# Kernel tuning notes

Measured on AMD Instinct MI355X. Metric: run time of the kernel, lower is better.

Reference implementation:

```python
import jax, jax.numpy as jnp
import numpy as np

B, T, D, E = 4, 2048, 1024, 8


def setup_inputs() -> dict:
    key = jax.random.key(0)
    ks = jax.random.split(key, 8)
    scale_g = float(np.sqrt(2.0 / (D + E)))  # xavier_uniform-ish scale for W_g
    scale_w = float(1.0 / np.sqrt(D))
    return {
        "x": jax.random.normal(ks[0], (B, T, D), dtype=jnp.float32),
        "noise": jax.random.normal(ks[1], (B, T, E), dtype=jnp.float32),  # the N(0,1) sample in Gating.forward
        "W_g": jax.random.normal(ks[2], (D, E), dtype=jnp.float32) * scale_g,
        "W_noise": jax.random.normal(ks[3], (D, E), dtype=jnp.float32),
        "W1": jax.random.normal(ks[4], (E, D, D), dtype=jnp.float32) * scale_w,
        "b1": jnp.zeros((E, D), dtype=jnp.float32),
        "W2": jax.random.normal(ks[5], (E, D, D), dtype=jnp.float32) * scale_w,
        "b2": jnp.zeros((E, D), dtype=jnp.float32),
        "k": 2,
    }


def _gates(x, noise, W_g, W_noise, k):
    # h = x@W_g + N(0,1) + softplus(x@W_noise)   (note: noise added, not scaled)
    h = jnp.einsum("btd,de->bte", x, W_g) + noise + jax.nn.softplus(
        jnp.einsum("btd,de->bte", x, W_noise)
    )
    kth = jax.lax.top_k(h, k)[0][..., -1:]           # kth largest per token
    h_masked = jnp.where(h >= kth, h, -jnp.inf)       # keepTopK (ties kept, as in torch)
    return jax.nn.softmax(h_masked, axis=-1)          # [B,T,E]


def reference(x, noise, W_g, W_noise, W1, b1, W2, b2, k):
    gates = _gates(x, noise, W_g, W_noise, k)
    # Dense loop over experts (faithful to original): every expert FFN on all tokens.
    # hidden: [E,B,T,D]
    hidden = jax.nn.relu(jnp.einsum("btd,edh->ebth", x, W1) + b1[:, None, None, :])
    expert_out = jnp.einsum("ebth,eho->ebto", hidden, W2) + b2[:, None, None, :]
    # mask-weighted combine: sum_e expert_out_e * gates[...,e]
    return jnp.einsum("ebtd,bte->btd", expert_out, gates)
```

## Files before the change

kernel.cpp:

```cpp
#include <hip/hip_runtime.h>
#include <hip/hip_bf16.h>

#define BTOK 8192
#define DDIM 1024
#define NEXP 8

typedef unsigned short u16;
typedef unsigned int u32;
typedef __attribute__((ext_vector_type(8))) short short8;
typedef __attribute__((ext_vector_type(4))) float f32x4;

constexpr int BM = 128, BN = 128, BK = 64;
constexpr int SLOTCAP = 3072;
constexpr int NT = DDIM / BK;

__device__ __forceinline__ u16 f2bf(float f){
  __hip_bfloat16 h = __float2bfloat16(f);
  return *reinterpret_cast<u16*>(&h);
}
__device__ __forceinline__ float bf2f(u16 v){
  return __uint_as_float(((u32)v) << 16);
}
__device__ __forceinline__ void gll16(const u16* gsrc, u16* ldst){
  __builtin_amdgcn_global_load_lds((const __attribute__((address_space(1))) void*)gsrc,
                                   (__attribute__((address_space(3))) void*)ldst,
                                   16, 0, 0);
}

#define GTOK 16
__global__ __launch_bounds__(512) void gating_kernel(
    const float* __restrict__ x, const float* __restrict__ noise,
    const float* __restrict__ Wg, const float* __restrict__ Wn,
    const int* __restrict__ kp,
    float* __restrict__ gates, int* __restrict__ counts, int* __restrict__ lists,
    int* __restrict__ tokmap, int* __restrict__ ncnt)
{
  __shared__ float lw[2][NEXP][4][260];
  __shared__ float lh[GTOK][NEXP];
  const int tid = threadIdx.x;

  for (int i = tid; i < 2*DDIM*NEXP; i += 512){
    const int mat = i >> 13;
    const int r   = i & 8191;
    const int d = r >> 3, ee = r & 7;
    const float* W = mat ? Wn : Wg;
    lw[mat][ee][d >> 8][d & 255] = W[r];
  }
  __syncthreads();

  const int q   = tid & 3;
  const int e   = (tid >> 2) & 7;
  const int tok = tid >> 5;
  const int t   = blockIdx.x * GTOK + tok;

  const float4* x4 = reinterpret_cast<const float4*>(x + (size_t)t*DDIM + q*256);
  const float4* g4 = reinterpret_cast<const float4*>(&lw[0][e][q][0]);
  const float4* n4 = reinterpret_cast<const float4*>(&lw[1][e][q][0]);
  float ag = 0.f, an = 0.f;
  #pragma unroll 8
  for (int j = 0; j < 64; ++j){
    const float4 xv = x4[j];
    const float4 wg = g4[j];
    const float4 wn = n4[j];
    ag = fmaf(xv.x,wg.x,fmaf(xv.y,wg.y,fmaf(xv.z,wg.z,fmaf(xv.w,wg.w,ag))));
    an = fmaf(xv.x,wn.x,fmaf(xv.y,wn.y,fmaf(xv.z,wn.z,fmaf(xv.w,wn.w,an))));
  }
  ag += __shfl_xor(ag, 1); an += __shfl_xor(an, 1);
  ag += __shfl_xor(ag, 2); an += __shfl_xor(an, 2);
  if (q == 0){
    const float sp = (an > 20.f) ? an : log1pf(expf(an));
    lh[tok][e] = ag + noise[(size_t)t*NEXP + e] + sp;
  }
  __syncthreads();
  if (tid < GTOK){
    const int tt = blockIdx.x * GTOK + tid;
    float h[NEXP];
    #pragma unroll
    for (int ee=0; ee<NEXP; ee++) h[ee] = lh[tid][ee];
    int kk = *kp; kk = kk<1?1:(kk>NEXP?NEXP:kk);
    bool used[NEXP];
    for (int ee=0; ee<NEXP; ee++) used[ee]=false;
    float kth = 0.f;
    for (int i2=0;i2<kk;i2++){
      int bi=0; float bv=-3.4e38f;
      for (int ee=0; ee<NEXP; ee++) if (!used[ee] && h[ee]>bv){bv=h[ee]; bi=ee;}
      used[bi]=true; kth=bv;
    }
    float m=-3.4e38f;
    for (int ee=0; ee<NEXP; ee++) if (h[ee]>=kth && h[ee]>m) m=h[ee];
    float p[NEXP], s=0.f;
    for (int ee=0; ee<NEXP; ee++){ p[ee]=(h[ee]>=kth)?expf(h[ee]-m):0.f; s+=p[ee]; }
    const float inv = 1.f/s;
    int nsel = 0;
    for (int ee=0; ee<NEXP; ee++){
      const float g = p[ee]*inv;
      gates[(size_t)tt*NEXP+ee] = g;
      if (g > 0.f){
        const int slot = atomicAdd(&counts[ee], 1);
        lists[ee*BTOK + slot] = tt;
        tokmap[tt*NEXP + nsel] = (ee << 13) | (slot & 8191);
        nsel++;
      }
    }
    ncnt[tt] = nsel;
  }
}

__global__ __launch_bounds__(256) void cast_x_kernel(const float4* __restrict__ x4,
                                                     ushort4* __restrict__ xb4)
{
  const int i = blockIdx.x*256 + threadIdx.x;
  const float4 v = x4[i];
  xb4[i] = make_ushort4(f2bf(v.x), f2bf(v.y), f2bf(v.z), f2bf(v.w));
}

__global__ __launch_bounds__(256) void trans_kernel(
    const float* __restrict__ W1, const float* __restrict__ W2,
    u16* __restrict__ W1T, u16* __restrict__ W2T)
{
  __shared__ float tile[64][65];
  const int mz = blockIdx.z;
  const float* src = (mz < NEXP) ? (W1  + (size_t)mz*DDIM*DDIM) : (W2  + (size_t)(mz-NEXP)*DDIM*DDIM);
  u16*       dst = (mz < NEXP) ? (W1T + (size_t)mz*DDIM*DDIM) : (W2T + (size_t)(mz-NEXP)*DDIM*DDIM);
  const int r0 = blockIdx.x*64, c0 = blockIdx.y*64;
  const int tx = threadIdx.x & 63, ty = threadIdx.x >> 6;
  #pragma unroll
  for (int i=ty;i<64;i+=4)
    tile[i][tx] = src[(size_t)(r0+i)*DDIM + c0+tx];
  __syncthreads();
  #pragma unroll
  for (int i=ty;i<64;i+=4)
    dst[(size_t)(c0+i)*DDIM + r0+tx] = f2bf(tile[tx][i]);
}

template<int LAYER>
__device__ __forceinline__ void ffn_body(
    const u16* __restrict__ Asrc, const u16* __restrict__ WT,
    const float* __restrict__ bias,
    const int* __restrict__ counts, const int* __restrict__ lists,
    u16* __restrict__ dst)
{
  const int e  = blockIdx.z;
  int cnt = counts[e]; if (cnt > SLOTCAP) cnt = SLOTCAP;
  const int m0 = blockIdx.x*BM;
  if (m0 >= cnt) return;
  const int n0 = blockIdx.y*BN;

  __shared__ __align__(16) u16 ldsA[2][BM*BK];
  __shared__ __align__(16) u16 ldsB[2][BN*BK];

  const int tid = threadIdx.x;
  const int wave = tid>>6, lane = tid&63;
  const int wm = wave>>1, wn = wave&1;

  const u16* aSrc[4]; const u16* bSrc[4];
  {
    const int lr = lane>>3, sp = lane&7;
    #pragma unroll
    for (int i=0;i<4;i++){
      const int row = wave*32 + i*8 + lr;
      const int ku  = sp ^ (row&7);
      size_t abase;
      if constexpr (LAYER==1){
        int gr = m0 + row; if (gr >= cnt) gr = cnt-1;
        const int tok = lists[e*BTOK + gr];
        abase = (size_t)tok * DDIM;
      } else {
        abase = ((size_t)e*SLOTCAP + m0 + row) * DDIM;
      }
      aSrc[i] = Asrc + abase + ku*8;
      bSrc[i] = WT + ((size_t)e*DDIM + n0 + row)*DDIM + ku*8;
    }
  }

  const int q = lane>>4, l16 = lane&15;
  int aoff[2][4], boff[2][4];
  #pragma unroll
  for (int f=0;f<4;f++){
    const int ra = wm*64 + f*16 + l16;
    const int rb = wn*64 + f*16 + l16;
    #pragma unroll
    for (int kk=0;kk<2;kk++){
      aoff[kk][f] = ra*BK + (((kk*4+q) ^ (ra&7))*8);
      boff[kk][f] = rb*BK + (((kk*4+q) ^ (rb&7))*8);
    }
  }

  f32x4 acc[4][4];
  #pragma unroll
  for (int i=0;i<4;i++)
    #pragma unroll
    for (int j=0;j<4;j++)
      acc[i][j] = (f32x4){0.f,0.f,0.f,0.f};

  #pragma unroll
  for (int i=0;i<4;i++){
    gll16(aSrc[i], &ldsA[0][(wave*4+i)*512]);
    gll16(bSrc[i], &ldsB[0][(wave*4+i)*512]);
  }
  __syncthreads();

  int cur = 0;
  for (int kt = 0; kt < NT-1; ++kt){
    #pragma unroll
    for (int i=0;i<4;i++){
      gll16(aSrc[i] + (size_t)(kt+1)*BK, &ldsA[cur^1][(wave*4+i)*512]);
      gll16(bSrc[i] + (size_t)(kt+1)*BK, &ldsB[cur^1][(wave*4+i)*512]);
    }
    #pragma unroll
    for (int kk=0;kk<2;kk++){
      short8 af[4], bfv[4];
      #pragma unroll
      for (int f=0;f<4;f++) af[f]  = *reinterpret_cast<const short8*>(&ldsA[cur][aoff[kk][f]]);
      #pragma unroll
      for (int f=0;f<4;f++) bfv[f] = *reinterpret_cast<const short8*>(&ldsB[cur][boff[kk][f]]);
      #pragma unroll
      for (int fm=0;fm<4;fm++)
        #pragma unroll
        for (int fn=0;fn<4;fn++)
          acc[fm][fn] = __builtin_amdgcn_mfma_f32_16x16x32_bf16(af[fm], bfv[fn], acc[fm][fn], 0, 0, 0);
    }
    __syncthreads();
    cur ^= 1;
  }
  #pragma unroll
  for (int kk=0;kk<2;kk++){
    short8 af[4], bfv[4];
    #pragma unroll
    for (int f=0;f<4;f++) af[f]  = *reinterpret_cast<const short8*>(&ldsA[cur][aoff[kk][f]]);
    #pragma unroll
    for (int f=0;f<4;f++) bfv[f] = *reinterpret_cast<const short8*>(&ldsB[cur][boff[kk][f]]);
    #pragma unroll
    for (int fm=0;fm<4;fm++)
      #pragma unroll
      for (int fn=0;fn<4;fn++)
        acc[fm][fn] = __builtin_amdgcn_mfma_f32_16x16x32_bf16(af[fm], bfv[fn], acc[fm][fn], 0, 0, 0);
  }

  #pragma unroll
  for (int fm=0;fm<4;fm++){
    #pragma unroll
    for (int r=0;r<4;r++){
      const int row = wm*64 + fm*16 + q*4 + r;
      const int gr  = m0 + row;
      #pragma unroll
      for (int fn=0;fn<4;fn++){
        const int col = n0 + wn*64 + fn*16 + l16;
        float v = acc[fm][fn][r] + bias[e*DDIM + col];
        if constexpr (LAYER==1) v = v > 0.f ? v : 0.f;
        dst[((size_t)e*SLOTCAP + gr)*DDIM + col] = f2bf(v);
      }
    }
  }
}

__global__ __launch_bounds__(256) void ffn1_kernel(
    const u16* __restrict__ A, const u16* __restrict__ WT, const float* __restrict__ b,
    const int* __restrict__ counts, const int* __restrict__ lists, u16* __restrict__ dst)
{ ffn_body<1>(A, WT, b, counts, lists, dst); }

__global__ __launch_bounds__(256) void ffn2_kernel(
    const u16* __restrict__ A, const u16* __restrict__ WT, const float* __restrict__ b,
    const int* __restrict__ counts, const int* __restrict__ lists, u16* __restrict__ dst)
{ ffn_body<2>(A, WT, b, counts, lists, dst); }

__global__ __launch_bounds__(256) void combine_kernel(
    const u16* __restrict__ partial, const int* __restrict__ tokmap,
    const int* __restrict__ ncnt, const float* __restrict__ gates,
    float* __restrict__ out)
{
  const int t = blockIdx.x, c = threadIdx.x;
  const int n = ncnt[t];
  float4 acc = {0.f, 0.f, 0.f, 0.f};
  for (int j = 0; j < n; ++j){
    const int ent  = tokmap[t*NEXP + j];
    const int e    = ent >> 13, slot = ent & 8191;
    if (slot >= SLOTCAP) continue;
    const float g = gates[(size_t)t*NEXP + e];
    const ushort4 pv = reinterpret_cast<const ushort4*>(
        partial + ((size_t)e*SLOTCAP + slot)*DDIM)[c];
    acc.x = fmaf(g, bf2f(pv.x), acc.x);
    acc.y = fmaf(g, bf2f(pv.y), acc.y);
    acc.z = fmaf(g, bf2f(pv.z), acc.z);
    acc.w = fmaf(g, bf2f(pv.w), acc.w);
  }
  reinterpret_cast<float4*>(out + (size_t)t*DDIM)[c] = acc;
}

extern "C" void kernel_launch(void* const* d_in, const int* in_sizes, int n_in,
                              void* d_out, int out_size, void* d_ws, size_t ws_size,
                              hipStream_t stream)
{
  const float* x     = (const float*)d_in[0];
  const float* noise = (const float*)d_in[1];
  const float* Wg    = (const float*)d_in[2];
  const float* Wn    = (const float*)d_in[3];
  const float* W1    = (const float*)d_in[4];
  const float* b1    = (const float*)d_in[5];
  const float* W2    = (const float*)d_in[6];
  const float* b2    = (const float*)d_in[7];
  const int*   kp    = (const int*)d_in[8];
  float* out = (float*)d_out;

  char* ws = (char*)d_ws;
  int*   counts = (int*)ws;
  int*   lists  = (int*)(ws + 4096);
  float* gates  = (float*)(ws + 266240);
  int*   tokmap = (int*)(ws + 528384);
  int*   ncnt   = (int*)(ws + 790528);
  u16*   xb     = (u16*)(ws + 1048576);
  u16*   W1T    = (u16*)(ws + 17825792);
  u16*   W2T    = (u16*)(ws + 34603008);
  u16*   hidden = (u16*)(ws + 51380224);
  u16*   partial= (u16*)(ws + 101711872);
  const size_t NEED = 152043520ull;

  hipMemsetAsync(counts, 0, 64, stream);
  if (ws_size < NEED){
    hipMemsetAsync(d_out, 0, (size_t)out_size*sizeof(float), stream);
    return;
  }

  cast_x_kernel<<<BTOK*DDIM/4/256, 256, 0, stream>>>((const float4*)x, (ushort4*)xb);
  trans_kernel<<<dim3(16,16,16), 256, 0, stream>>>(W1, W2, W1T, W2T);
  gating_kernel<<<BTOK/GTOK, 512, 0, stream>>>(x, noise, Wg, Wn, kp,
                                               gates, counts, lists, tokmap, ncnt);
  ffn1_kernel<<<dim3(SLOTCAP/BM, DDIM/BN, NEXP), 256, 0, stream>>>(
      xb, W1T, b1, counts, lists, hidden);
  ffn2_kernel<<<dim3(SLOTCAP/BM, DDIM/BN, NEXP), 256, 0, stream>>>(
      hidden, W2T, b2, counts, lists, partial);
  combine_kernel<<<BTOK, 256, 0, stream>>>(partial, tokmap, ncnt, gates, out);
}
```

Before: 366.6 us.

## Fuse bf16 cast of x into gating, split selection into block-aggregated kernel

The fp32-to-bf16 cast of x moves into the gating score kernel, so x is read from global memory once instead of twice, and one launch is removed. Top-k selection and slot assignment move to a separate kernel with one token per thread. Slots are counted first with shared-memory atomics and then reserved with one global atomic per expert per block. The gating dot products also use split accumulators for more ILP. In exchange there is an extra launch, a small h buffer round trip, and a divergent bf16 store done only by the e==0 lanes.

```diff
diff --git a/kernel.cpp b/kernel.cpp
--- a/kernel.cpp
+++ b/kernel.cpp
@@ -28,15 +28,12 @@
 }
 
 #define GTOK 16
-__global__ __launch_bounds__(512) void gating_kernel(
+__global__ __launch_bounds__(512) void gating_score_kernel(
     const float* __restrict__ x, const float* __restrict__ noise,
     const float* __restrict__ Wg, const float* __restrict__ Wn,
-    const int* __restrict__ kp,
-    float* __restrict__ gates, int* __restrict__ counts, int* __restrict__ lists,
-    int* __restrict__ tokmap, int* __restrict__ ncnt)
+    float* __restrict__ h_out, u16* __restrict__ xb)
 {
   __shared__ float lw[2][NEXP][4][260];
-  __shared__ float lh[GTOK][NEXP];
   const int tid = threadIdx.x;
 
   for (int i = tid; i < 2*DDIM*NEXP; i += 512){
@@ -56,62 +53,87 @@
   const float4* x4 = reinterpret_cast<const float4*>(x + (size_t)t*DDIM + q*256);
   const float4* g4 = reinterpret_cast<const float4*>(&lw[0][e][q][0]);
   const float4* n4 = reinterpret_cast<const float4*>(&lw[1][e][q][0]);
-  float ag = 0.f, an = 0.f;
+  ushort4* xb4 = reinterpret_cast<ushort4*>(xb + (size_t)t*DDIM + q*256);
+  float agx=0.f, agz=0.f, anx=0.f, anz=0.f;
   #pragma unroll 8
   for (int j = 0; j < 64; ++j){
     const float4 xv = x4[j];
     const float4 wg = g4[j];
     const float4 wn = n4[j];
-    ag = fmaf(xv.x,wg.x,fmaf(xv.y,wg.y,fmaf(xv.z,wg.z,fmaf(xv.w,wg.w,ag))));
-    an = fmaf(xv.x,wn.x,fmaf(xv.y,wn.y,fmaf(xv.z,wn.z,fmaf(xv.w,wn.w,an))));
-  }
+    agx = fmaf(xv.x,wg.x, fmaf(xv.y,wg.y, agx));
+    agz = fmaf(xv.z,wg.z, fmaf(xv.w,wg.w, agz));
+    anx = fmaf(xv.x,wn.x, fmaf(xv.y,wn.y, anx));
+    anz = fmaf(xv.z,wn.z, fmaf(xv.w,wn.w, anz));
+    if (e == 0)
+      xb4[j] = make_ushort4(f2bf(xv.x), f2bf(xv.y), f2bf(xv.z), f2bf(xv.w));
+  }
+  float ag = agx + agz, an = anx + anz;
   ag += __shfl_xor(ag, 1); an += __shfl_xor(an, 1);
   ag += __shfl_xor(ag, 2); an += __shfl_xor(an, 2);
   if (q == 0){
     const float sp = (an > 20.f) ? an : log1pf(expf(an));
-    lh[tok][e] = ag + noise[(size_t)t*NEXP + e] + sp;
-  }
-  __syncthreads();
-  if (tid < GTOK){
-    const int tt = blockIdx.x * GTOK + tid;
-    float h[NEXP];
-    #pragma unroll
-    for (int ee=0; ee<NEXP; ee++) h[ee] = lh[tid][ee];
-    int kk = *kp; kk = kk<1?1:(kk>NEXP?NEXP:kk);
-    bool used[NEXP];
-    for (int ee=0; ee<NEXP; ee++) used[ee]=false;
-    float kth = 0.f;
-    for (int i2=0;i2<kk;i2++){
-      int bi=0; float bv=-3.4e38f;
-      for (int ee=0; ee<NEXP; ee++) if (!used[ee] && h[ee]>bv){bv=h[ee]; bi=ee;}
-      used[bi]=true; kth=bv;
-    }
-    float m=-3.4e38f;
-    for (int ee=0; ee<NEXP; ee++) if (h[ee]>=kth && h[ee]>m) m=h[ee];
-    float p[NEXP], s=0.f;
-    for (int ee=0; ee<NEXP; ee++){ p[ee]=(h[ee]>=kth)?expf(h[ee]-m):0.f; s+=p[ee]; }
-    const float inv = 1.f/s;
-    int nsel = 0;
-    for (int ee=0; ee<NEXP; ee++){
-      const float g = p[ee]*inv;
-      gates[(size_t)tt*NEXP+ee] = g;
-      if (g > 0.f){
-        const int slot = atomicAdd(&counts[ee], 1);
-        lists[ee*BTOK + slot] = tt;
-        tokmap[tt*NEXP + nsel] = (ee << 13) | (slot & 8191);
-        nsel++;
-      }
-    }
-    ncnt[tt] = nsel;
-  }
-}
-
-__global__ __launch_bounds__(256) void cast_x_kernel(const float4* __restrict__ x4,
-                                                     ushort4* __restrict__ xb4)
-{
-  const int i = blockIdx.x*256 + threadIdx.x;
-  const float4 v = x4[i];
-  xb4[i] = make_ushort4(f2bf(v.x), f2bf(v.y), f2bf(v.z), f2bf(v.w));
+    h_out[(size_t)t*NEXP + e] = ag + noise[(size_t)t*NEXP + e] + sp;
+  }
+}
+
+__global__ __launch_bounds__(256) void gating_select_kernel(
+    const float* __restrict__ h_in, const int* __restrict__ kp,
+    float* __restrict__ gates, int* __restrict__ counts, int* __restrict__ lists,
+    int* __restrict__ tokmap, int* __restrict__ ncnt)
+{
+  __shared__ int lcnt[NEXP];
+  __shared__ int lbase[NEXP];
+  const int tid = threadIdx.x;
+  const int t   = blockIdx.x*256 + tid;
+  if (tid < NEXP) lcnt[tid] = 0;
+  __syncthreads();
+
+  float h[NEXP];
+  const float4 h0 = reinterpret_cast<const float4*>(h_in + (size_t)t*NEXP)[0];
+  const float4 h1 = reinterpret_cast<const float4*>(h_in + (size_t)t*NEXP)[1];
+  h[0]=h0.x; h[1]=h0.y; h[2]=h0.z; h[3]=h0.w;
+  h[4]=h1.x; h[5]=h1.y; h[6]=h1.z; h[7]=h1.w;
+
+  int kk = *kp; kk = kk<1?1:(kk>NEXP?NEXP:kk);
+  bool used[NEXP];
+  #pragma unroll
+  for (int e=0;e<NEXP;e++) used[e]=false;
+  float kth = 0.f;
+  for (int i=0;i<kk;i++){
+    int bi=0; float bv=-3.4e38f;
+    #pragma unroll
+    for (int e=0;e<NEXP;e++) if (!used[e] && h[e]>bv){bv=h[e]; bi=e;}
+    used[bi]=true; kth=bv;
+  }
+  float m=-3.4e38f;
+  #pragma unroll
+  for (int e=0;e<NEXP;e++) if (h[e]>=kth && h[e]>m) m=h[e];
+  float p[NEXP], s=0.f;
+  #pragma unroll
+  for (int e=0;e<NEXP;e++){ p[e]=(h[e]>=kth)?expf(h[e]-m):0.f; s+=p[e]; }
+  const float inv = 1.f/s;
+  float g[NEXP];
+  int lslot[NEXP];
+  #pragma unroll
+  for (int e=0;e<NEXP;e++){
+    g[e] = p[e]*inv;
+    gates[(size_t)t*NEXP + e] = g[e];
+    if (g[e] > 0.f) lslot[e] = atomicAdd(&lcnt[e], 1);
+  }
+  __syncthreads();
+  if (tid < NEXP) lbase[tid] = atomicAdd(&counts[tid], lcnt[tid]);
+  __syncthreads();
+  int idx = 0;
+  #pragma unroll
+  for (int e=0;e<NEXP;e++){
+    if (g[e] > 0.f){
+      const int slot = lbase[e] + lslot[e];
+      lists[e*BTOK + slot] = t;
+      tokmap[t*NEXP + idx] = (e << 13) | (slot & 8191);
+      idx++;
+    }
+  }
+  ncnt[t] = idx;
 }
 
 __global__ __launch_bounds__(256) void trans_kernel(
@@ -308,12 +330,13 @@
   float* gates  = (float*)(ws + 266240);
   int*   tokmap = (int*)(ws + 528384);
   int*   ncnt   = (int*)(ws + 790528);
-  u16*   xb     = (u16*)(ws + 1048576);
-  u16*   W1T    = (u16*)(ws + 17825792);
-  u16*   W2T    = (u16*)(ws + 34603008);
-  u16*   hidden = (u16*)(ws + 51380224);
-  u16*   partial= (u16*)(ws + 101711872);
-  const size_t NEED = 152043520ull;
+  float* hbuf   = (float*)(ws + 823296);
+  u16*   xb     = (u16*)(ws + 1085440);
+  u16*   W1T    = (u16*)(ws + 17862656);
+  u16*   W2T    = (u16*)(ws + 34639872);
+  u16*   hidden = (u16*)(ws + 51417088);
+  u16*   partial= (u16*)(ws + 101748736);
+  const size_t NEED = 152080384ull;
 
   hipMemsetAsync(counts, 0, 64, stream);
   if (ws_size < NEED){
@@ -321,10 +344,10 @@
     return;
   }
 
-  cast_x_kernel<<<BTOK*DDIM/4/256, 256, 0, stream>>>((const float4*)x, (ushort4*)xb);
   trans_kernel<<<dim3(16,16,16), 256, 0, stream>>>(W1, W2, W1T, W2T);
-  gating_kernel<<<BTOK/GTOK, 512, 0, stream>>>(x, noise, Wg, Wn, kp,
-                                               gates, counts, lists, tokmap, ncnt);
+  gating_score_kernel<<<BTOK/GTOK, 512, 0, stream>>>(x, noise, Wg, Wn, hbuf, xb);
+  gating_select_kernel<<<BTOK/256, 256, 0, stream>>>(hbuf, kp, gates, counts, lists,
+                                                     tokmap, ncnt);
   ffn1_kernel<<<dim3(SLOTCAP/BM, DDIM/BN, NEXP), 256, 0, stream>>>(
       xb, W1T, b1, counts, lists, hidden);
   ffn2_kernel<<<dim3(SLOTCAP/BM, DDIM/BN, NEXP), 256, 0, stream>>>(
```

After: 330.5 us. 1.11x faster.
